# Kernel optimization log

Measured on AMD Instinct MI355X. Metric: run time of the kernel, lower is better.

Reference implementation:

```python
import jax, jax.numpy as jnp
import numpy as np

N_NODES = 100_000
N_EDGES = 1_600_000
N_TOKENS = 16
VOCAB = 32_000
TOK_DIM = 64
NODE_DIM = 64
HID = 128
FC = 128
NUM_GRAPHS = 1024


def setup_inputs() -> dict:
    key = jax.random.key(0)
    ks = jax.random.split(key, 14)
    emb = jax.random.normal(ks[0], (VOCAB, TOK_DIM), jnp.float32) * 0.02
    emb = emb.at[0].set(0.0)  # padding_idx=0 row is zero
    return {
        "x_token_idxs": jax.random.randint(ks[1], (N_NODES, N_TOKENS), 0, VOCAB),
        "edge_index": jax.random.randint(ks[2], (2, N_EDGES), 0, N_NODES),
        "batch": jnp.sort(jax.random.randint(ks[3], (N_NODES,), 0, NUM_GRAPHS)),
        "emb": emb,
        "Wp": jax.random.normal(ks[4], (TOK_DIM, NODE_DIM), jnp.float32) * (1.0 / np.sqrt(TOK_DIM)),
        "bp": jnp.zeros((NODE_DIM,), jnp.float32),
        "W1": jax.random.normal(ks[5], (NODE_DIM, HID), jnp.float32) * (1.0 / np.sqrt(NODE_DIM)),
        "b1": jnp.zeros((HID,), jnp.float32),
        "W2": jax.random.normal(ks[6], (HID, HID), jnp.float32) * (1.0 / np.sqrt(HID)),
        "b2": jnp.zeros((HID,), jnp.float32),
        "Wfc": jax.random.normal(ks[7], (HID, FC), jnp.float32) * (1.0 / np.sqrt(HID)),
        "bfc": jnp.zeros((FC,), jnp.float32),
        "Wout": jax.random.normal(ks[8], (FC, 1), jnp.float32) * (1.0 / np.sqrt(FC)),
        "bout": jnp.zeros((1,), jnp.float32),
    }


def reference(x_token_idxs, edge_index, batch, emb, Wp, bp, W1, b1, W2, b2, Wfc, bfc, Wout, bout):
    N = x_token_idxs.shape[0]
    # token embed -> mean pool over tokens -> node projection
    node = emb[x_token_idxs].mean(axis=1) @ Wp + bp  # [N, NODE_DIM]

    # GCN normalization with self-loops (PyG gcn_norm, symmetric)
    loops = jnp.arange(N)
    src = jnp.concatenate([edge_index[0], loops])
    dst = jnp.concatenate([edge_index[1], loops])
    deg = jax.ops.segment_sum(jnp.ones_like(dst, jnp.float32), dst, num_segments=N)
    dis = jnp.where(deg > 0, jax.lax.rsqrt(deg), 0.0)
    norm = (dis[src] * dis[dst])[:, None]  # [E+N, 1]

    def gcn(x, W, b):
        h = x @ W                                      # linear transform first (in->out)
        msg = h[src] * norm                            # gather + scale
        return jax.ops.segment_sum(msg, dst, num_segments=N) + b  # scatter-add + bias

    x = jax.nn.relu(gcn(node, W1, b1))
    x = jax.nn.relu(gcn(x, W2, b2))

    # global mean pool by graph id
    cnt = jax.ops.segment_sum(jnp.ones((N,), jnp.float32), batch, num_segments=NUM_GRAPHS)
    g = jax.ops.segment_sum(x, batch, num_segments=NUM_GRAPHS) / jnp.maximum(cnt, 1.0)[:, None]

    g = jax.nn.relu(g @ Wfc + bfc)
    logits = (g @ Wout + bout).squeeze(-1)  # [NUM_GRAPHS]
    return jax.nn.sigmoid(logits), logits
```

## Files before the change

### kernel.cpp

```cpp
#include <hip/hip_runtime.h>
#include <hip/hip_bf16.h>
#include <hip/hip_fp16.h>
#include <math.h>

#define N_TOKENS 16
#define TOK_DIM 64
#define NODE_DIM 64
#define HID 128
#define FC 128
#define NUM_GRAPHS 1024
#define NBUCK_MAX 512
#define CHUNK 8192

typedef _Float16 f16x8 __attribute__((ext_vector_type(8)));
typedef float f32x4 __attribute__((ext_vector_type(4)));

__device__ __forceinline__ __half2 shfl_xor_h2(__half2 v, int mask) {
    int i = *(int*)&v;
    i = __shfl_xor(i, mask);
    return *(__half2*)&i;
}

__global__ void prep_fused_kernel(const float* __restrict__ Wp, const float* __restrict__ W1,
                                  const float* __restrict__ W2, const float* __restrict__ bp,
                                  const float* __restrict__ emb,
                                  _Float16* __restrict__ Wf16t, _Float16* __restrict__ W2t,
                                  float* __restrict__ bf, __half* __restrict__ emb16, int n4) {
    int b = blockIdx.x;
    int t = threadIdx.x;
    if (b < 128) {
        int n = b;
        if (t < 64) {
            float acc = 0.f;
#pragma unroll
            for (int d = 0; d < 64; d++) acc += Wp[t * 64 + d] * W1[d * 128 + n];
            Wf16t[(size_t)n * 64 + t] = (_Float16)acc;
        } else if (t < 128) {
            int d = t - 64;
            float v = bp[d] * W1[d * 128 + n];
#pragma unroll
            for (int off = 32; off > 0; off >>= 1) v += __shfl_down(v, off);
            if (d == 0) bf[n] = v;
        }
        if (t < 128) W2t[(size_t)n * 128 + t] = (_Float16)W2[(size_t)t * 128 + n];
    } else {
        int i = (b - 128) * 256 + t;
        if (i < n4) {
            float4 v = ((const float4*)emb)[i];
            __half2 h0 = __floats2half2_rn(v.x, v.y);
            __half2 h1 = __floats2half2_rn(v.z, v.w);
            float2 p;
            ((__half2*)&p)[0] = h0;
            ((__half2*)&p)[1] = h1;
            ((float2*)emb16)[i] = p;
        }
    }
}

__global__ void embed_mean_kernel(const int* __restrict__ tok,
                                  const __half* __restrict__ emb16,
                                  __half* __restrict__ mean16, int N) {
    int t = threadIdx.x;
    int w = t >> 6, j = t & 63;
    int q = j >> 3, l = j & 7;
    int i = blockIdx.x * 4 + w;
    if (i >= N) return;
    const float4* e4 = (const float4*)emb16;
    int t0 = tok[i * 16 + q];
    int t1 = tok[i * 16 + q + 8];
    float4 v0 = e4[(size_t)t0 * 8 + l];
    float4 v1 = e4[(size_t)t1 * 8 + l];
    const __half2* p0 = (const __half2*)&v0;
    const __half2* p1 = (const __half2*)&v1;
    __half2 a0 = __hadd2(p0[0], p1[0]);
    __half2 a1 = __hadd2(p0[1], p1[1]);
    __half2 a2 = __hadd2(p0[2], p1[2]);
    __half2 a3 = __hadd2(p0[3], p1[3]);
#pragma unroll
    for (int mask = 8; mask <= 32; mask <<= 1) {
        a0 = __hadd2(a0, shfl_xor_h2(a0, mask));
        a1 = __hadd2(a1, shfl_xor_h2(a1, mask));
        a2 = __hadd2(a2, shfl_xor_h2(a2, mask));
        a3 = __hadd2(a3, shfl_xor_h2(a3, mask));
    }
    if (q == 0) {
        __half2 inv = __floats2half2_rn(1.0f / 16.0f, 1.0f / 16.0f);
        float4 packed;
        __half2* pp = (__half2*)&packed;
        pp[0] = __hmul2(a0, inv);
        pp[1] = __hmul2(a1, inv);
        pp[2] = __hmul2(a2, inv);
        pp[3] = __hmul2(a3, inv);
        ((float4*)mean16)[(size_t)i * 8 + l] = packed;
    }
}

__global__ void bucket_hist_kernel(const int* __restrict__ dst, int* __restrict__ hist2d,
                                   int E, int nbuck) {
    __shared__ int h[NBUCK_MAX];
    int t = threadIdx.x;
    for (int i = t; i < nbuck; i += 512) h[i] = 0;
    __syncthreads();
    int base = blockIdx.x * CHUNK;
    for (int i = t; i < CHUNK; i += 512) {
        int e = base + i;
        if (e < E) atomicAdd(&h[dst[e] >> 8], 1);
    }
    __syncthreads();
    int* row = hist2d + (size_t)blockIdx.x * NBUCK_MAX;
    for (int i = t; i < nbuck; i += 512) row[i] = h[i];
}

__global__ void chunk_scan_kernel(const int* __restrict__ hist2d, int* __restrict__ chunkbase,
                                  int* __restrict__ total, int nchunk) {
    int b = blockIdx.x;
    int lane = threadIdx.x;
    int run = 0;
    for (int c0 = 0; c0 < nchunk; c0 += 64) {
        int c = c0 + lane;
        int v = (c < nchunk) ? hist2d[(size_t)c * NBUCK_MAX + b] : 0;
        int s = v;
#pragma unroll
        for (int off = 1; off < 64; off <<= 1) {
            int u = __shfl_up(s, off);
            if (lane >= off) s += u;
        }
        if (c < nchunk) chunkbase[(size_t)c * NBUCK_MAX + b] = s - v + run;
        run += __shfl(s, 63);
    }
    if (lane == 0) total[b] = run;
}

__global__ void bucket_scan_kernel(const int* __restrict__ total,
                                   int* __restrict__ bucket_base, int nbuck) {
    __shared__ int s[512];
    int tid = threadIdx.x;
    int v = (tid < nbuck) ? total[tid] : 0;
    s[tid] = v;
    __syncthreads();
    for (int off = 1; off < 512; off <<= 1) {
        int add = (tid >= off) ? s[tid - off] : 0;
        __syncthreads();
        s[tid] += add;
        __syncthreads();
    }
    if (tid < nbuck) bucket_base[tid] = s[tid] - v;
    if (tid == 511) bucket_base[nbuck] = s[511];
}

__global__ void binscatter_kernel(const int* __restrict__ src, const int* __restrict__ dst,
                                  const int* __restrict__ bucket_base,
                                  const int* __restrict__ chunkbase,
                                  int* __restrict__ staged, int E, int nbuck) {
    __shared__ int h[NBUCK_MAX];
    int t = threadIdx.x;
    const int* cb = chunkbase + (size_t)blockIdx.x * NBUCK_MAX;
    for (int i = t; i < nbuck; i += 512) h[i] = bucket_base[i] + cb[i];
    __syncthreads();
    int base = blockIdx.x * CHUNK;
    for (int i = t; i < CHUNK; i += 512) {
        int e = base + i;
        if (e < E) {
            int d = dst[e], s = src[e];
            int b = d >> 8;
            int r = atomicAdd(&h[b], 1);
            staged[r] = s | ((d & 255) << 17);
        }
    }
}

__global__ void bucket_count_kernel(const int* __restrict__ staged,
                                    const int* __restrict__ bucket_base,
                                    int* __restrict__ row_start, float* __restrict__ dis,
                                    int N, int E) {
    __shared__ int cnt[256];
    __shared__ int sc[256];
    int b = blockIdx.x;
    int t = threadIdx.x;
    cnt[t] = 0;
    __syncthreads();
    int rb0 = bucket_base[b], rb1 = bucket_base[b + 1];
    for (int i = rb0 + t; i < rb1; i += 256) atomicAdd(&cnt[staged[i] >> 17], 1);
    __syncthreads();
    int v = cnt[t];
    sc[t] = v;
    __syncthreads();
    for (int off = 1; off < 256; off <<= 1) {
        int add = (t >= off) ? sc[t - off] : 0;
        __syncthreads();
        sc[t] += add;
        __syncthreads();
    }
    int node = b * 256 + t;
    if (node < N) {
        row_start[node] = rb0 + sc[t] - v;
        dis[node] = rsqrtf(1.0f + (float)v);
    }
    if (b == 0 && t == 0) row_start[N] = E;
}

__global__ void csr_write_kernel(const int* __restrict__ staged,
                                 const int* __restrict__ bucket_base,
                                 const int* __restrict__ row_start,
                                 const float* __restrict__ dis,
                                 int2* __restrict__ csr, float* __restrict__ rowsum, int N) {
    __shared__ int cur[256];
    __shared__ float dl[256];
    __shared__ float wsum[256];
    int b = blockIdx.x;
    int t = threadIdx.x;
    int node = b * 256 + t;
    cur[t] = (node < N) ? row_start[node] : 0;
    dl[t] = (node < N) ? dis[node] : 0.f;
    wsum[t] = 0.f;
    __syncthreads();
    int rb0 = bucket_base[b], rb1 = bucket_base[b + 1];
    for (int i = rb0 + t; i < rb1; i += 256) {
        int v = staged[i];
        int s = v & 131071;
        int dloc = v >> 17;
        float w = dis[s] * dl[dloc];
        int pos = atomicAdd(&cur[dloc], 1);
        __half2 wh = __floats2half2_rn(w, w);
        csr[pos] = make_int2(s, *(int*)&wh);
        atomicAdd(&wsum[dloc], w);
    }
    __syncthreads();
    if (node < N) rowsum[node] = wsum[t] + dl[t] * dl[t];
}

#define NB 32
__global__ __launch_bounds__(256, 6)
void agg64_dense_kernel(const __half* __restrict__ mean16,
                        const int* __restrict__ row_start,
                        const int2* __restrict__ csr,
                        const float* __restrict__ dis,
                        const float* __restrict__ rowsum,
                        const _Float16* __restrict__ Wf16t,
                        const float* __restrict__ bf,
                        const float* __restrict__ b1,
                        const _Float16* __restrict__ W2t,
                        __half* __restrict__ h2, int N) {
    __shared__ _Float16 sagg[32][72];
    __shared__ _Float16 sx1[32][136];
    __shared__ float srs[32];
    int t = threadIdx.x;
    int w = t >> 6, j = t & 63;
    int q = j >> 3, l = j & 7;
    int nb0 = blockIdx.x * NB;
    const float4* m4 = (const float4*)mean16;

    if (t < 32) srs[t] = (nb0 + t < N) ? rowsum[nb0 + t] : 0.f;

    for (int s = 0; s < 8; s++) {
        int node = nb0 + w * 8 + s;
        __half2 a0, a1, a2, a3;
        a0 = a1 = a2 = a3 = __floats2half2_rn(0.f, 0.f);
        if (node < N) {
            int beg = row_start[node];
            int end = row_start[node + 1];
            float d = dis[node];
            {
                float4 raw = m4[(size_t)node * 8 + l];
                const __half2* hp = (const __half2*)&raw;
                float d2f = d * d * ((q == 0) ? 1.f : 0.f);
                __half2 d2h = __floats2half2_rn(d2f, d2f);
                a0 = __hmul2(hp[0], d2h); a1 = __hmul2(hp[1], d2h);
                a2 = __hmul2(hp[2], d2h); a3 = __hmul2(hp[3], d2h);
            }
            int k = beg;
            int kfull = beg + ((end - beg) & ~31);
            for (; k < kfull; k += 32) {
                int2 e[4];
                float4 v[4];
#pragma unroll
                for (int m = 0; m < 4; m++) e[m] = csr[k + 8 * m + q];
#pragma unroll
                for (int m = 0; m < 4; m++) v[m] = m4[(size_t)e[m].x * 8 + l];
#pragma unroll
                for (int m = 0; m < 4; m++) {
                    __half2 wh = *(__half2*)&e[m].y;
                    const __half2* hp = (const __half2*)&v[m];
                    a0 = __hfma2(hp[0], wh, a0);
                    a1 = __hfma2(hp[1], wh, a1);
                    a2 = __hfma2(hp[2], wh, a2);
                    a3 = __hfma2(hp[3], wh, a3);
                }
            }
            if (k < end) {
                int2 e[4];
                float4 v[4];
#pragma unroll
                for (int m = 0; m < 4; m++) {
                    int kk = k + 8 * m + q;
                    e[m] = (kk < end) ? csr[kk] : make_int2(0, 0);
                }
#pragma unroll
                for (int m = 0; m < 4; m++) v[m] = m4[(size_t)e[m].x * 8 + l];
#pragma unroll
                for (int m = 0; m < 4; m++) {
                    __half2 wh = *(__half2*)&e[m].y;
                    const __half2* hp = (const __half2*)&v[m];
                    a0 = __hfma2(hp[0], wh, a0);
                    a1 = __hfma2(hp[1], wh, a1);
                    a2 = __hfma2(hp[2], wh, a2);
                    a3 = __hfma2(hp[3], wh, a3);
                }
            }
        }
#pragma unroll
        for (int mask = 8; mask <= 32; mask <<= 1) {
            a0 = __hadd2(a0, shfl_xor_h2(a0, mask));
            a1 = __hadd2(a1, shfl_xor_h2(a1, mask));
            a2 = __hadd2(a2, shfl_xor_h2(a2, mask));
            a3 = __hadd2(a3, shfl_xor_h2(a3, mask));
        }
        if (q == 0) {
            float4 packed;
            __half2* pp = (__half2*)&packed;
            pp[0] = a0; pp[1] = a1; pp[2] = a2; pp[3] = a3;
            *(float4*)(&sagg[w * 8 + s][l * 8]) = packed;
        }
    }
    __syncthreads();

    int wv = w, lane = j;
    int rh = wv & 1;
    int ncb = (wv >> 1) * 64;
    int m16 = lane & 15;
    int qq = lane >> 4;

    f32x4 c0 = {}, c1 = {}, c2 = {}, c3 = {};
#pragma unroll
    for (int ks = 0; ks < 2; ks++) {
        int k0 = ks * 32 + qq * 8;
        f16x8 afrag = *(const f16x8*)(&sagg[rh * 16 + m16][k0]);
        f16x8 b0 = *(const f16x8*)(Wf16t + (size_t)(ncb + 0 * 16 + m16) * 64 + k0);
        f16x8 b1f = *(const f16x8*)(Wf16t + (size_t)(ncb + 1 * 16 + m16) * 64 + k0);
        f16x8 b2f = *(const f16x8*)(Wf16t + (size_t)(ncb + 2 * 16 + m16) * 64 + k0);
        f16x8 b3f = *(const f16x8*)(Wf16t + (size_t)(ncb + 3 * 16 + m16) * 64 + k0);
        c0 = __builtin_amdgcn_mfma_f32_16x16x32_f16(afrag, b0, c0, 0, 0, 0);
        c1 = __builtin_amdgcn_mfma_f32_16x16x32_f16(afrag, b1f, c1, 0, 0, 0);
        c2 = __builtin_amdgcn_mfma_f32_16x16x32_f16(afrag, b2f, c2, 0, 0, 0);
        c3 = __builtin_amdgcn_mfma_f32_16x16x32_f16(afrag, b3f, c3, 0, 0, 0);
    }
    {
        f32x4 cc[4] = {c0, c1, c2, c3};
#pragma unroll
        for (int nt = 0; nt < 4; nt++) {
            int ncol = ncb + nt * 16 + m16;
            float bfj = bf[ncol], b1j = b1[ncol];
#pragma unroll
            for (int r = 0; r < 4; r++) {
                int mrow = qq * 4 + r;
                float z = cc[nt][r] + srs[rh * 16 + mrow] * bfj + b1j;
                sx1[rh * 16 + mrow][ncol] = (_Float16)fmaxf(z, 0.f);
            }
        }
    }
    __syncthreads();

    f32x4 d0 = {}, d1 = {}, d2 = {}, d3 = {};
#pragma unroll
    for (int ks = 0; ks < 4; ks++) {
        int k0 = ks * 32 + qq * 8;
        f16x8 afrag = *(const f16x8*)(&sx1[rh * 16 + m16][k0]);
        f16x8 b0 = *(const f16x8*)(W2t + (size_t)(ncb + 0 * 16 + m16) * 128 + k0);
        f16x8 b1f = *(const f16x8*)(W2t + (size_t)(ncb + 1 * 16 + m16) * 128 + k0);
        f16x8 b2f = *(const f16x8*)(W2t + (size_t)(ncb + 2 * 16 + m16) * 128 + k0);
        f16x8 b3f = *(const f16x8*)(W2t + (size_t)(ncb + 3 * 16 + m16) * 128 + k0);
        d0 = __builtin_amdgcn_mfma_f32_16x16x32_f16(afrag, b0, d0, 0, 0, 0);
        d1 = __builtin_amdgcn_mfma_f32_16x16x32_f16(afrag, b1f, d1, 0, 0, 0);
        d2 = __builtin_amdgcn_mfma_f32_16x16x32_f16(afrag, b2f, d2, 0, 0, 0);
        d3 = __builtin_amdgcn_mfma_f32_16x16x32_f16(afrag, b3f, d3, 0, 0, 0);
    }
    {
        f32x4 dd[4] = {d0, d1, d2, d3};
#pragma unroll
        for (int nt = 0; nt < 4; nt++) {
            int ncol = ncb + nt * 16 + m16;
#pragma unroll
            for (int r = 0; r < 4; r++) {
                int node = nb0 + rh * 16 + qq * 4 + r;
                if (node < N) h2[(size_t)node * 128 + ncol] = __float2half(dd[nt][r]);
            }
        }
    }
}

__global__ __launch_bounds__(256, 8)
void gcn_agg128_kernel(const __half* __restrict__ hsrc,
                       const int* __restrict__ row_start,
                       const int2* __restrict__ csr,
                       const float* __restrict__ dis,
                       const float* __restrict__ b2,
                       __half* __restrict__ outx, int N) {
    int t = threadIdx.x;
    int w = t >> 6, j = t & 63;
    int q = j >> 4, l = j & 15;
    int node = blockIdx.x * 4 + w;
    if (node >= N) return;
    const float4* h4 = (const float4*)hsrc;
    int beg = row_start[node];
    int end = row_start[node + 1];
    float d = dis[node];
    __half2 a0, a1, a2, a3;
    {
        float4 raw = h4[(size_t)node * 16 + l];
        const __half2* hp = (const __half2*)&raw;
        float d2f = d * d * ((q == 0) ? 1.f : 0.f);
        __half2 d2h = __floats2half2_rn(d2f, d2f);
        a0 = __hmul2(hp[0], d2h); a1 = __hmul2(hp[1], d2h);
        a2 = __hmul2(hp[2], d2h); a3 = __hmul2(hp[3], d2h);
    }
    int k = beg;
    int kfull = beg + ((end - beg) & ~31);
    for (; k < kfull; k += 32) {
        int2 e[8];
        float4 v[8];
#pragma unroll
        for (int m = 0; m < 8; m++) e[m] = csr[k + 4 * m + q];
#pragma unroll
        for (int m = 0; m < 8; m++) v[m] = h4[(size_t)e[m].x * 16 + l];
#pragma unroll
        for (int m = 0; m < 8; m++) {
            __half2 wh = *(__half2*)&e[m].y;
            const __half2* hp = (const __half2*)&v[m];
            a0 = __hfma2(hp[0], wh, a0);
            a1 = __hfma2(hp[1], wh, a1);
            a2 = __hfma2(hp[2], wh, a2);
            a3 = __hfma2(hp[3], wh, a3);
        }
    }
    if (k < end) {
        int2 e[8];
        float4 v[8];
#pragma unroll
        for (int m = 0; m < 8; m++) {
            int kk = k + 4 * m + q;
            e[m] = (kk < end) ? csr[kk] : make_int2(0, 0);
        }
#pragma unroll
        for (int m = 0; m < 8; m++) v[m] = h4[(size_t)e[m].x * 16 + l];
#pragma unroll
        for (int m = 0; m < 8; m++) {
            __half2 wh = *(__half2*)&e[m].y;
            const __half2* hp = (const __half2*)&v[m];
            a0 = __hfma2(hp[0], wh, a0);
            a1 = __hfma2(hp[1], wh, a1);
            a2 = __hfma2(hp[2], wh, a2);
            a3 = __hfma2(hp[3], wh, a3);
        }
    }
#pragma unroll
    for (int mask = 16; mask <= 32; mask <<= 1) {
        a0 = __hadd2(a0, shfl_xor_h2(a0, mask));
        a1 = __hadd2(a1, shfl_xor_h2(a1, mask));
        a2 = __hadd2(a2, shfl_xor_h2(a2, mask));
        a3 = __hadd2(a3, shfl_xor_h2(a3, mask));
    }
    if (q == 0) {
        float2 f0 = __half22float2(a0), f1 = __half22float2(a1);
        float2 f2 = __half22float2(a2), f3 = __half22float2(a3);
        const float4* b4 = (const float4*)b2;
        float4 ba = b4[l * 2], bb = b4[l * 2 + 1];
        __half2 o0 = __floats2half2_rn(fmaxf(f0.x + ba.x, 0.f), fmaxf(f0.y + ba.y, 0.f));
        __half2 o1 = __floats2half2_rn(fmaxf(f1.x + ba.z, 0.f), fmaxf(f1.y + ba.w, 0.f));
        __half2 o2 = __floats2half2_rn(fmaxf(f2.x + bb.x, 0.f), fmaxf(f2.y + bb.y, 0.f));
        __half2 o3 = __floats2half2_rn(fmaxf(f3.x + bb.z, 0.f), fmaxf(f3.y + bb.w, 0.f));
        float4 packed;
        __half2* pp = (__half2*)&packed;
        pp[0] = o0; pp[1] = o1; pp[2] = o2; pp[3] = o3;
        ((float4*)outx)[(size_t)node * 16 + l] = packed;
    }
}

__device__ __forceinline__ int lower_bound_i(const int* __restrict__ a, int n, int val) {
    int lo = 0, hi = n;
    while (lo < hi) {
        int mid = (lo + hi) >> 1;
        if (a[mid] < val) lo = mid + 1; else hi = mid;
    }
    return lo;
}

__global__ void pool_head_kernel(const __half* __restrict__ x,
                                 const int* __restrict__ batch,
                                 const float* __restrict__ Wfc,
                                 const float* __restrict__ bfc,
                                 const float* __restrict__ Wout,
                                 const float* __restrict__ bout,
                                 float* __restrict__ out, int N) {
    int gr = blockIdx.x;
    int t = threadIdx.x;
    int j2 = t & 63, w = t >> 6;
    __shared__ float2 spart[4][64];
    __shared__ float sg[128];
    __shared__ float sfc[2][128];
    __shared__ float sred[128];
    int beg = lower_bound_i(batch, N, gr);
    int end = lower_bound_i(batch, N, gr + 1);
    const __half2* x2 = (const __half2*)x;
    float2 acc = make_float2(0.f, 0.f);
    for (int i = beg + w; i < end; i += 4) {
        float2 a = __half22float2(x2[(size_t)i * 64 + j2]);
        acc.x += a.x; acc.y += a.y;
    }
    spart[w][j2] = acc;
    __syncthreads();
    if (t < 64) {
        float inv = 1.0f / fmaxf((float)(end - beg), 1.0f);
        float2 s0 = spart[0][t], s1 = spart[1][t];
        float2 s2 = spart[2][t], s3 = spart[3][t];
        sg[2 * t] = (s0.x + s1.x + s2.x + s3.x) * inv;
        sg[2 * t + 1] = (s0.y + s1.y + s2.y + s3.y) * inv;
    }
    __syncthreads();
    int j = t & 127, hb = t >> 7;
    float a = 0.f;
#pragma unroll
    for (int k = 0; k < 64; k++) a += sg[hb * 64 + k] * Wfc[(hb * 64 + k) * 128 + j];
    sfc[hb][j] = a;
    __syncthreads();
    if (t < 128) {
        float aa = sfc[0][t] + sfc[1][t] + bfc[t];
        float f = fmaxf(aa, 0.f);
        sred[t] = f * Wout[t];
    }
    __syncthreads();
    if (t < 64) {
        float v = sred[t] + sred[t + 64];
#pragma unroll
        for (int off = 32; off > 0; off >>= 1) v += __shfl_down(v, off);
        if (t == 0) {
            float logit = v + bout[0];
            out[gr] = 1.0f / (1.0f + expf(-logit));
            out[NUM_GRAPHS + gr] = logit;
        }
    }
}

extern "C" void kernel_launch(void* const* d_in, const int* in_sizes, int n_in,
                              void* d_out, int out_size, void* d_ws, size_t ws_size,
                              hipStream_t stream) {
    const int* tok   = (const int*)d_in[0];
    const int* eidx  = (const int*)d_in[1];
    const int* batch = (const int*)d_in[2];
    const float* emb = (const float*)d_in[3];
    const float* Wp  = (const float*)d_in[4];
    const float* bp  = (const float*)d_in[5];
    const float* W1  = (const float*)d_in[6];
    const float* b1  = (const float*)d_in[7];
    const float* W2  = (const float*)d_in[8];
    const float* b2  = (const float*)d_in[9];
    const float* Wfc = (const float*)d_in[10];
    const float* bfc = (const float*)d_in[11];
    const float* Wout= (const float*)d_in[12];
    const float* bout= (const float*)d_in[13];
    float* out = (float*)d_out;

    const int N = in_sizes[2];
    const int E = in_sizes[1] / 2;
    const int* src = eidx;
    const int* dst = eidx + E;
    const int Np = (N + 3) & ~3;
    const int nbuck = (N + 255) / 256;
    const int nchunk = (E + CHUNK - 1) / CHUNK;
    const int emb_n4 = in_sizes[3] / 4;

    float* ws = (float*)d_ws;
    size_t off = 0;
    float* dis     = ws + off;            off += Np;
    __half* mean16 = (__half*)(ws + off); off += (size_t)Np * 32;
    __half* agg16  = (__half*)(ws + off); off += (size_t)Np * 32;
    float* rowsum  = ws + off;            off += Np;
    __half* h2buf  = (__half*)(ws + off); off += (size_t)Np * 64;
    __half* xfin16 = (__half*)(ws + off); off += (size_t)Np * 64;
    __half* emb16  = (__half*)(ws + off); off += (size_t)(in_sizes[3] / 2 + 4);
    _Float16* Wf16t = (_Float16*)(ws + off); off += 4096;
    _Float16* W2t   = (_Float16*)(ws + off); off += 8192;
    float* bf      = ws + off;            off += 128;
    int* row_start = (int*)(ws + off);    off += Np + 4;
    int* staged    = (int*)(ws + off);    off += E;
    int* total     = (int*)(ws + off);    off += NBUCK_MAX;
    int* bucket_base   = (int*)(ws + off); off += NBUCK_MAX + 8;
    int2* csr      = (int2*)(ws + off);
    int* hist2d    = (int*)h2buf;
    int* chunkbase = hist2d + (size_t)nchunk * NBUCK_MAX;

    prep_fused_kernel<<<128 + (emb_n4 + 255) / 256, 256, 0, stream>>>(
        Wp, W1, W2, bp, emb, Wf16t, W2t, bf, emb16, emb_n4);

    bucket_hist_kernel<<<nchunk, 512, 0, stream>>>(dst, hist2d, E, nbuck);
    chunk_scan_kernel<<<nbuck, 64, 0, stream>>>(hist2d, chunkbase, total, nchunk);
    bucket_scan_kernel<<<1, 512, 0, stream>>>(total, bucket_base, nbuck);
    binscatter_kernel<<<nchunk, 512, 0, stream>>>(src, dst, bucket_base, chunkbase,
                                                  staged, E, nbuck);
    bucket_count_kernel<<<nbuck, 256, 0, stream>>>(staged, bucket_base, row_start, dis, N, E);
    csr_write_kernel<<<nbuck, 256, 0, stream>>>(staged, bucket_base, row_start, dis,
                                                csr, rowsum, N);

    embed_mean_kernel<<<(N + 3) / 4, 256, 0, stream>>>(tok, emb16, mean16, N);

    agg64_dense_kernel<<<(N + NB - 1) / NB, 256, 0, stream>>>(mean16, row_start, csr, dis,
                                                              rowsum, Wf16t, bf, b1, W2t,
                                                              h2buf, N);

    gcn_agg128_kernel<<<(N + 3) / 4, 256, 0, stream>>>(h2buf, row_start, csr, dis, b2,
                                                       xfin16, N);

    pool_head_kernel<<<NUM_GRAPHS, 256, 0, stream>>>(xfin16, batch, Wfc, bfc, Wout, bout,
                                                     out, N);
}
```

Before: 317.0 us.

## Assign one wave per node in layer-1 aggregation with 8-node blocks

The fused layer-1 aggregate plus dense kernel now uses 512-thread blocks covering 8 nodes, one wavefront per node, instead of 256-thread blocks where each wave processed 8 nodes serially. The MFMA stage uses one 16-column tile per wave with half the A rows zero-padded. The aim is more parallelism and latency hiding in the irregular gather. In exchange, half of each MFMA is wasted and weight fragments are re-read from global memory four times as often per node.

```diff
diff --git a/kernel.cpp b/kernel.cpp
--- a/kernel.cpp
+++ b/kernel.cpp
@@ -229,8 +229,8 @@
     if (node < N) rowsum[node] = wsum[t] + dl[t] * dl[t];
 }
 
-#define NB 32
-__global__ __launch_bounds__(256, 6)
+#define NB8 8
+__global__ __launch_bounds__(512, 8)
 void agg64_dense_kernel(const __half* __restrict__ mean16,
                         const int* __restrict__ row_start,
                         const int2* __restrict__ csr,
@@ -241,25 +241,24 @@
                         const float* __restrict__ b1,
                         const _Float16* __restrict__ W2t,
                         __half* __restrict__ h2, int N) {
-    __shared__ _Float16 sagg[32][72];
-    __shared__ _Float16 sx1[32][136];
-    __shared__ float srs[32];
-    int t = threadIdx.x;
-    int w = t >> 6, j = t & 63;
-    int q = j >> 3, l = j & 7;
-    int nb0 = blockIdx.x * NB;
+    __shared__ _Float16 sagg[8][72];
+    __shared__ _Float16 sx1[8][136];
+    __shared__ float srs[8];
+    int t = threadIdx.x;
+    int wv = t >> 6, j = t & 63;
+    int nb0 = blockIdx.x * NB8;
     const float4* m4 = (const float4*)mean16;
 
-    if (t < 32) srs[t] = (nb0 + t < N) ? rowsum[nb0 + t] : 0.f;
-
-    for (int s = 0; s < 8; s++) {
-        int node = nb0 + w * 8 + s;
-        __half2 a0, a1, a2, a3;
-        a0 = a1 = a2 = a3 = __floats2half2_rn(0.f, 0.f);
+    if (t < 8) srs[t] = (nb0 + t < N) ? rowsum[nb0 + t] : 0.f;
+
+    {
+        int q = j >> 3, l = j & 7;
+        int node = nb0 + wv;
         if (node < N) {
             int beg = row_start[node];
             int end = row_start[node + 1];
             float d = dis[node];
+            __half2 a0, a1, a2, a3;
             {
                 float4 raw = m4[(size_t)node * 8 + l];
                 const __half2* hp = (const __half2*)&raw;
@@ -307,84 +306,62 @@
                     a3 = __hfma2(hp[3], wh, a3);
                 }
             }
-        }
-#pragma unroll
-        for (int mask = 8; mask <= 32; mask <<= 1) {
-            a0 = __hadd2(a0, shfl_xor_h2(a0, mask));
-            a1 = __hadd2(a1, shfl_xor_h2(a1, mask));
-            a2 = __hadd2(a2, shfl_xor_h2(a2, mask));
-            a3 = __hadd2(a3, shfl_xor_h2(a3, mask));
-        }
-        if (q == 0) {
-            float4 packed;
-            __half2* pp = (__half2*)&packed;
-            pp[0] = a0; pp[1] = a1; pp[2] = a2; pp[3] = a3;
-            *(float4*)(&sagg[w * 8 + s][l * 8]) = packed;
-        }
-    }
-    __syncthreads();
-
-    int wv = w, lane = j;
-    int rh = wv & 1;
-    int ncb = (wv >> 1) * 64;
-    int m16 = lane & 15;
-    int qq = lane >> 4;
-
-    f32x4 c0 = {}, c1 = {}, c2 = {}, c3 = {};
+#pragma unroll
+            for (int mask = 8; mask <= 32; mask <<= 1) {
+                a0 = __hadd2(a0, shfl_xor_h2(a0, mask));
+                a1 = __hadd2(a1, shfl_xor_h2(a1, mask));
+                a2 = __hadd2(a2, shfl_xor_h2(a2, mask));
+                a3 = __hadd2(a3, shfl_xor_h2(a3, mask));
+            }
+            if (q == 0) {
+                float4 packed;
+                __half2* pp = (__half2*)&packed;
+                pp[0] = a0; pp[1] = a1; pp[2] = a2; pp[3] = a3;
+                *(float4*)(&sagg[wv][l * 8]) = packed;
+            }
+        }
+    }
+    __syncthreads();
+
+    int m16 = j & 15, qq = j >> 4;
+    int ncol = wv * 16 + m16;
+
+    f32x4 c = {};
 #pragma unroll
     for (int ks = 0; ks < 2; ks++) {
         int k0 = ks * 32 + qq * 8;
-        f16x8 afrag = *(const f16x8*)(&sagg[rh * 16 + m16][k0]);
-        f16x8 b0 = *(const f16x8*)(Wf16t + (size_t)(ncb + 0 * 16 + m16) * 64 + k0);
-        f16x8 b1f = *(const f16x8*)(Wf16t + (size_t)(ncb + 1 * 16 + m16) * 64 + k0);
-        f16x8 b2f = *(const f16x8*)(Wf16t + (size_t)(ncb + 2 * 16 + m16) * 64 + k0);
-        f16x8 b3f = *(const f16x8*)(Wf16t + (size_t)(ncb + 3 * 16 + m16) * 64 + k0);
-        c0 = __builtin_amdgcn_mfma_f32_16x16x32_f16(afrag, b0, c0, 0, 0, 0);
-        c1 = __builtin_amdgcn_mfma_f32_16x16x32_f16(afrag, b1f, c1, 0, 0, 0);
-        c2 = __builtin_amdgcn_mfma_f32_16x16x32_f16(afrag, b2f, c2, 0, 0, 0);
-        c3 = __builtin_amdgcn_mfma_f32_16x16x32_f16(afrag, b3f, c3, 0, 0, 0);
+        f16x8 afrag = {};
+        if (m16 < 8) afrag = *(const f16x8*)(&sagg[m16][k0]);
+        f16x8 bfrag = *(const f16x8*)(Wf16t + (size_t)ncol * 64 + k0);
+        c = __builtin_amdgcn_mfma_f32_16x16x32_f16(afrag, bfrag, c, 0, 0, 0);
     }
     {
-        f32x4 cc[4] = {c0, c1, c2, c3};
-#pragma unroll
-        for (int nt = 0; nt < 4; nt++) {
-            int ncol = ncb + nt * 16 + m16;
-            float bfj = bf[ncol], b1j = b1[ncol];
-#pragma unroll
-            for (int r = 0; r < 4; r++) {
-                int mrow = qq * 4 + r;
-                float z = cc[nt][r] + srs[rh * 16 + mrow] * bfj + b1j;
-                sx1[rh * 16 + mrow][ncol] = (_Float16)fmaxf(z, 0.f);
+        float bfj = bf[ncol], b1j = b1[ncol];
+#pragma unroll
+        for (int r = 0; r < 4; r++) {
+            int mrow = qq * 4 + r;
+            if (mrow < 8) {
+                float z = c[r] + srs[mrow] * bfj + b1j;
+                sx1[mrow][ncol] = (_Float16)fmaxf(z, 0.f);
             }
         }
     }
     __syncthreads();
 
-    f32x4 d0 = {}, d1 = {}, d2 = {}, d3 = {};
+    f32x4 dd = {};
 #pragma unroll
     for (int ks = 0; ks < 4; ks++) {
         int k0 = ks * 32 + qq * 8;
-        f16x8 afrag = *(const f16x8*)(&sx1[rh * 16 + m16][k0]);
-        f16x8 b0 = *(const f16x8*)(W2t + (size_t)(ncb + 0 * 16 + m16) * 128 + k0);
-        f16x8 b1f = *(const f16x8*)(W2t + (size_t)(ncb + 1 * 16 + m16) * 128 + k0);
-        f16x8 b2f = *(const f16x8*)(W2t + (size_t)(ncb + 2 * 16 + m16) * 128 + k0);
-        f16x8 b3f = *(const f16x8*)(W2t + (size_t)(ncb + 3 * 16 + m16) * 128 + k0);
-        d0 = __builtin_amdgcn_mfma_f32_16x16x32_f16(afrag, b0, d0, 0, 0, 0);
-        d1 = __builtin_amdgcn_mfma_f32_16x16x32_f16(afrag, b1f, d1, 0, 0, 0);
-        d2 = __builtin_amdgcn_mfma_f32_16x16x32_f16(afrag, b2f, d2, 0, 0, 0);
-        d3 = __builtin_amdgcn_mfma_f32_16x16x32_f16(afrag, b3f, d3, 0, 0, 0);
-    }
-    {
-        f32x4 dd[4] = {d0, d1, d2, d3};
-#pragma unroll
-        for (int nt = 0; nt < 4; nt++) {
-            int ncol = ncb + nt * 16 + m16;
-#pragma unroll
-            for (int r = 0; r < 4; r++) {
-                int node = nb0 + rh * 16 + qq * 4 + r;
-                if (node < N) h2[(size_t)node * 128 + ncol] = __float2half(dd[nt][r]);
-            }
-        }
+        f16x8 afrag = {};
+        if (m16 < 8) afrag = *(const f16x8*)(&sx1[m16][k0]);
+        f16x8 bfrag = *(const f16x8*)(W2t + (size_t)ncol * 128 + k0);
+        dd = __builtin_amdgcn_mfma_f32_16x16x32_f16(afrag, bfrag, dd, 0, 0, 0);
+    }
+#pragma unroll
+    for (int r = 0; r < 4; r++) {
+        int mrow = qq * 4 + r;
+        int node = nb0 + mrow;
+        if (mrow < 8 && node < N) h2[(size_t)node * 128 + ncol] = __float2half(dd[r]);
     }
 }
 
@@ -602,9 +579,9 @@
 
     embed_mean_kernel<<<(N + 3) / 4, 256, 0, stream>>>(tok, emb16, mean16, N);
 
-    agg64_dense_kernel<<<(N + NB - 1) / NB, 256, 0, stream>>>(mean16, row_start, csr, dis,
-                                                              rowsum, Wf16t, bf, b1, W2t,
-                                                              h2buf, N);
+    agg64_dense_kernel<<<(N + NB8 - 1) / NB8, 512, 0, stream>>>(mean16, row_start, csr, dis,
+                                                                rowsum, Wf16t, bf, b1, W2t,
+                                                                h2buf, N);
 
     gcn_agg128_kernel<<<(N + 3) / 4, 256, 0, stream>>>(h2buf, row_start, csr, dis, b2,
                                                        xfin16, N);
```

Result: slower. 346.3 us (+9.3%).
